# Optimization experiments

Measured on AMD Instinct MI355X. Metric: run time of the kernel, lower is better.

Reference implementation:

```python
import jax, jax.numpy as jnp
import numpy as np

EPS = 1e-12  # torch F.normalize clamps the norm at 1e-12

def _l2norm(v, axis):
    n = jnp.sqrt(jnp.sum(v * v, axis=axis, keepdims=True))
    return v / jnp.maximum(n, EPS)

def setup_inputs() -> dict:
    key = jax.random.key(0)
    k1, k2, k3, k4 = jax.random.split(key, 4)
    N, C, H, W, K = 64, 64, 64, 64, 128
    alpha = 1.0
    x = jax.random.normal(k1, (N, C, H, W), dtype=jnp.float32)
    centroids = jax.random.uniform(k2, (K, C), dtype=jnp.float32)
    # conv is initialized from centroids (2*alpha*c, -alpha*||c||) but is an
    # independent parameter after init; keep the init relationship for realism.
    conv_w = 2.0 * alpha * centroids
    conv_b = -alpha * jnp.sqrt(jnp.sum(centroids * centroids, axis=1))
    return {"x": x, "centroids": centroids, "conv_w": conv_w, "conv_b": conv_b}

def reference(x, centroids, conv_w, conv_b):
    N, C, H, W = x.shape
    K = centroids.shape[0]
    # L2-normalize descriptors along channel dim
    xn = _l2norm(x, axis=1)                                   # [N,C,H,W]
    # 1x1 conv == per-pixel linear map C->K
    logits = jnp.einsum('nchw,kc->nkhw', xn, conv_w) + conv_b[None, :, None, None]
    sa = jax.nn.softmax(logits.reshape(N, K, H * W), axis=1)  # [N,K,HW]
    xf = xn.reshape(N, C, H * W)                              # [N,C,HW]
    # vlad[n,k,c] = sum_l sa[n,k,l] * (xf[n,c,l] - centroids[k,c])
    #            = (sa @ xf^T)[n,k,c] - sum_l sa[n,k,l] * centroids[k,c]
    vlad = jnp.einsum('nkl,ncl->nkc', sa, xf) - sa.sum(axis=-1)[:, :, None] * centroids[None]
    vlad = _l2norm(vlad, axis=2)            # intra-normalization per cluster
    vlad = vlad.reshape(N, K * C)
    vlad = _l2norm(vlad, axis=1)            # global L2 normalization
    return vlad
```

## Files before the change

### kernel.cpp

```cpp
#include <hip/hip_runtime.h>
#include <math.h>

#define NIMG   64
#define CDIM   64
#define HWPX   4096
#define PARTS  8
#define KCL    128
#define PIXPART (HWPX / PARTS)
#define TL     32
#define NCHUNK (PIXPART / TL)
#define SHIFT  10.0f

#define XP_S 72
#define XC_S 40
#define PH_S 40

typedef __attribute__((ext_vector_type(8))) short short8;
typedef __attribute__((ext_vector_type(4))) float f32x4;

#define MFMA(a, b, c) __builtin_amdgcn_mfma_f32_16x16x32_bf16((a), (b), (c), 0, 0, 0)

__device__ __forceinline__ void tsplit(float f, short& hs, short& ls) {
    unsigned u = __builtin_bit_cast(unsigned, f);
    hs = (short)(u >> 16);
    float hf = __builtin_bit_cast(float, u & 0xffff0000u);
    ls = (short)(__builtin_bit_cast(unsigned, f - hf) >> 16);
}

__global__ __launch_bounds__(256, 2)
void netvlad_main(const float* __restrict__ x,
                  const float* __restrict__ conv_w,
                  const float* __restrict__ conv_b,
                  float* __restrict__ vout,
                  float* __restrict__ asout,
                  int use_atomic)
{
    __shared__ __align__(16) short xp_hi[TL * XP_S],  xp_lo[TL * XP_S];
    __shared__ __align__(16) short xc_hi[CDIM * XC_S], xc_lo[CDIM * XC_S];
    __shared__ __align__(16) short ph_hi[KCL * PH_S],  ph_lo[KCL * PH_S];
    __shared__ __align__(16) float redA[TL * 4];
    __shared__ float sumP[4 * TL];

    const int t   = threadIdx.x;
    const int w   = t >> 6;
    const int l   = t & 63;
    const int l15 = l & 15, l4 = l >> 4;
    const int n    = blockIdx.x >> 3;
    const int part = blockIdx.x & 7;
    const int p_s  = t & 31;
    const int sg   = t >> 5;

    short8 wh[2][2], wl[2][2];
    #pragma unroll
    for (int kt = 0; kt < 2; ++kt) {
        const int krow = (2 * w + kt) * 16 + l15;
        #pragma unroll
        for (int ks = 0; ks < 2; ++ks) {
            const float4* wp = (const float4*)(conv_w + krow * CDIM + ks * 32 + l4 * 8);
            float4 wa = wp[0], wb = wp[1];
            float wv[8] = {wa.x, wa.y, wa.z, wa.w, wb.x, wb.y, wb.z, wb.w};
            #pragma unroll
            for (int j = 0; j < 8; ++j) {
                short hs, ls; tsplit(wv[j], hs, ls);
                wh[kt][ks][j] = hs; wl[kt][ks][j] = ls;
            }
        }
    }
    float cbr[2][4];
    #pragma unroll
    for (int kt = 0; kt < 2; ++kt)
        #pragma unroll
        for (int i = 0; i < 4; ++i)
            cbr[kt][i] = conv_b[(2 * w + kt) * 16 + l4 * 4 + i] - SHIFT;

    f32x4 acc2[2][4];
    #pragma unroll
    for (int a = 0; a < 2; ++a)
        #pragma unroll
        for (int b = 0; b < 4; ++b) acc2[a][b] = (f32x4)0.0f;
    float asr[2][4];
    #pragma unroll
    for (int a = 0; a < 2; ++a)
        #pragma unroll
        for (int i = 0; i < 4; ++i) asr[a][i] = 0.f;

    const float* xbase = x + (size_t)n * CDIM * HWPX + part * PIXPART;

    float xv[8];
    #pragma unroll
    for (int j = 0; j < 8; ++j)
        xv[j] = xbase[(sg * 8 + j) * HWPX + p_s];

    for (int ch = 0; ch < NCHUNK; ++ch) {
        float ssq = 0.f;
        #pragma unroll
        for (int j = 0; j < 8; ++j) ssq += xv[j] * xv[j];
        ssq += __shfl_xor(ssq, 32);
        if (l < 32) redA[p_s * 4 + w] = ssq;

        short8 vh, vl;
        #pragma unroll
        for (int j = 0; j < 8; ++j) {
            short hs, ls; tsplit(xv[j], hs, ls);
            vh[j] = hs; vl[j] = ls;
            xc_hi[(sg * 8 + j) * XC_S + p_s] = hs;
            xc_lo[(sg * 8 + j) * XC_S + p_s] = ls;
        }
        *(short8*)&xp_hi[p_s * XP_S + sg * 8] = vh;
        *(short8*)&xp_lo[p_s * XP_S + sg * 8] = vl;
        __syncthreads();

        if (ch + 1 < NCHUNK) {
            #pragma unroll
            for (int j = 0; j < 8; ++j)
                xv[j] = xbase[(sg * 8 + j) * HWPX + (ch + 1) * TL + p_s];
        }

        f32x4 a1[2][2];
        #pragma unroll
        for (int a = 0; a < 2; ++a)
            #pragma unroll
            for (int b = 0; b < 2; ++b) a1[a][b] = (f32x4)0.0f;
        #pragma unroll
        for (int ks = 0; ks < 2; ++ks) {
            #pragma unroll
            for (int pt = 0; pt < 2; ++pt) {
                short8 bh = *(short8*)&xp_hi[(pt * 16 + l15) * XP_S + ks * 32 + l4 * 8];
                short8 bl = *(short8*)&xp_lo[(pt * 16 + l15) * XP_S + ks * 32 + l4 * 8];
                #pragma unroll
                for (int kt = 0; kt < 2; ++kt) {
                    a1[kt][pt] = MFMA(wh[kt][ks], bh, a1[kt][pt]);
                    a1[kt][pt] = MFMA(wh[kt][ks], bl, a1[kt][pt]);
                    a1[kt][pt] = MFMA(wl[kt][ks], bh, a1[kt][pt]);
                }
            }
        }

        float rn[2];
        #pragma unroll
        for (int pt = 0; pt < 2; ++pt) {
            float4 r4 = *(const float4*)&redA[(pt * 16 + l15) * 4];
            rn[pt] = 1.0f / fmaxf(sqrtf((r4.x + r4.y) + (r4.z + r4.w)), 1e-12f);
        }

        float e[2][2][4], sp[2] = {0.f, 0.f};
        #pragma unroll
        for (int kt = 0; kt < 2; ++kt)
            #pragma unroll
            for (int pt = 0; pt < 2; ++pt)
                #pragma unroll
                for (int i = 0; i < 4; ++i) {
                    float ev = __expf(fmaf(a1[kt][pt][i], rn[pt], cbr[kt][i]));
                    e[kt][pt][i] = ev;
                    sp[pt] += ev;
                }
        #pragma unroll
        for (int pt = 0; pt < 2; ++pt) {
            sp[pt] += __shfl_xor(sp[pt], 16);
            sp[pt] += __shfl_xor(sp[pt], 32);
        }
        if (l4 == 0) {
            sumP[w * TL + l15]      = sp[0];
            sumP[w * TL + 16 + l15] = sp[1];
        }
        __syncthreads();

        float rden[2], rdn2[2];
        #pragma unroll
        for (int pt = 0; pt < 2; ++pt) {
            const int col = pt * 16 + l15;
            float den = sumP[col] + sumP[TL + col] + sumP[2 * TL + col] + sumP[3 * TL + col];
            rden[pt] = 1.0f / den;
            rdn2[pt] = rden[pt] * rn[pt];
        }

        #pragma unroll
        for (int kt = 0; kt < 2; ++kt)
            #pragma unroll
            for (int i = 0; i < 4; ++i) {
                const int row = (2 * w + kt) * 16 + l4 * 4 + i;
                #pragma unroll
                for (int pt = 0; pt < 2; ++pt) {
                    float ev = e[kt][pt][i];
                    asr[kt][i] = fmaf(ev, rden[pt], asr[kt][i]);
                    float Pn = ev * rdn2[pt];
                    short hs, ls; tsplit(Pn, hs, ls);
                    ph_hi[row * PH_S + pt * 16 + l15] = hs;
                    ph_lo[row * PH_S + pt * 16 + l15] = ls;
                }
            }
        __syncthreads();

        {
            short8 xh2[4], xl2[4];
            #pragma unroll
            for (int ct = 0; ct < 4; ++ct) {
                xh2[ct] = *(short8*)&xc_hi[(ct * 16 + l15) * XC_S + l4 * 8];
                xl2[ct] = *(short8*)&xc_lo[(ct * 16 + l15) * XC_S + l4 * 8];
            }
            #pragma unroll
            for (int kt = 0; kt < 2; ++kt) {
                short8 ah = *(short8*)&ph_hi[((2 * w + kt) * 16 + l15) * PH_S + l4 * 8];
                short8 al = *(short8*)&ph_lo[((2 * w + kt) * 16 + l15) * PH_S + l4 * 8];
                #pragma unroll
                for (int ct = 0; ct < 4; ++ct) {
                    acc2[kt][ct] = MFMA(ah, xh2[ct], acc2[kt][ct]);
                    acc2[kt][ct] = MFMA(ah, xl2[ct], acc2[kt][ct]);
                    acc2[kt][ct] = MFMA(al, xh2[ct], acc2[kt][ct]);
                }
            }
        }
        __syncthreads();
    }

    float* vg = use_atomic ? vout + (size_t)n * KCL * CDIM
                           : vout + (size_t)(n * PARTS + part) * KCL * CDIM;
    #pragma unroll
    for (int kt = 0; kt < 2; ++kt)
        #pragma unroll
        for (int ct = 0; ct < 4; ++ct)
            #pragma unroll
            for (int i = 0; i < 4; ++i) {
                const int row = (2 * w + kt) * 16 + l4 * 4 + i;
                const int col = ct * 16 + l15;
                if (use_atomic) atomicAdd(&vg[row * CDIM + col], acc2[kt][ct][i]);
                else            vg[row * CDIM + col] = acc2[kt][ct][i];
            }

    #pragma unroll
    for (int kt = 0; kt < 2; ++kt)
        #pragma unroll
        for (int i = 0; i < 4; ++i) {
            float v = asr[kt][i];
            v += __shfl_xor(v, 1); v += __shfl_xor(v, 2);
            v += __shfl_xor(v, 4); v += __shfl_xor(v, 8);
            if (l15 == 0) {
                const int row = (2 * w + kt) * 16 + l4 * 4 + i;
                if (use_atomic) atomicAdd(&asout[n * KCL + row], v);
                else            asout[(n * PARTS + part) * KCL + row] = v;
            }
        }
}

__global__ __launch_bounds__(1024)
void netvlad_finalize(const float* __restrict__ vpart,
                      const float* __restrict__ aspart,
                      const float* __restrict__ cent,
                      float* __restrict__ out,
                      int nparts)
{
    __shared__ float wred[16];
    __shared__ float gsh;

    const int t = threadIdx.x;
    const int n = blockIdx.x;
    const int k = t >> 3, c0 = (t & 7) * 8;
    const int w2 = t >> 6;

    float vsum[8];
    #pragma unroll
    for (int j = 0; j < 8; ++j) vsum[j] = 0.f;
    float av = 0.f;
    for (int pt = 0; pt < nparts; ++pt) {
        const float* vg = vpart + (((size_t)n * nparts + pt) * KCL + k) * CDIM + c0;
        float4 a = *(const float4*)&vg[0];
        float4 b = *(const float4*)&vg[4];
        vsum[0] += a.x; vsum[1] += a.y; vsum[2] += a.z; vsum[3] += a.w;
        vsum[4] += b.x; vsum[5] += b.y; vsum[6] += b.z; vsum[7] += b.w;
        av += aspart[(n * nparts + pt) * KCL + k];
    }

    const float* cg = cent + k * CDIM + c0;
    float4 ca = *(const float4*)&cg[0];
    float4 cb4 = *(const float4*)&cg[4];
    float cc[8] = {ca.x, ca.y, ca.z, ca.w, cb4.x, cb4.y, cb4.z, cb4.w};
    float ss = 0.f;
    #pragma unroll
    for (int j = 0; j < 8; ++j) {
        vsum[j] -= av * cc[j];
        ss += vsum[j] * vsum[j];
    }
    ss += __shfl_xor(ss, 1); ss += __shfl_xor(ss, 2); ss += __shfl_xor(ss, 4);
    const float rinv = 1.0f / fmaxf(sqrtf(ss), 1e-12f);

    float contrib = ss * rinv * rinv * 0.125f;
    #pragma unroll
    for (int off = 1; off < 64; off <<= 1) contrib += __shfl_xor(contrib, off);
    if ((t & 63) == 0) wred[w2] = contrib;
    __syncthreads();
    if (t == 0) {
        float g = 0.f;
        #pragma unroll
        for (int j = 0; j < 16; ++j) g += wred[j];
        gsh = 1.0f / fmaxf(sqrtf(g), 1e-12f);
    }
    __syncthreads();

    const float s = rinv * gsh;
    float* og = out + (size_t)n * KCL * CDIM + k * CDIM + c0;
    float4 o0, o1;
    o0.x = vsum[0] * s; o0.y = vsum[1] * s; o0.z = vsum[2] * s; o0.w = vsum[3] * s;
    o1.x = vsum[4] * s; o1.y = vsum[5] * s; o1.z = vsum[6] * s; o1.w = vsum[7] * s;
    *(float4*)&og[0] = o0;
    *(float4*)&og[4] = o1;
}

extern "C" void kernel_launch(void* const* d_in, const int* in_sizes, int n_in,
                              void* d_out, int out_size, void* d_ws, size_t ws_size,
                              hipStream_t stream) {
    const float* x     = (const float*)d_in[0];
    const float* cent  = (const float*)d_in[1];
    const float* convw = (const float*)d_in[2];
    const float* convb = (const float*)d_in[3];
    float* out = (float*)d_out;

    const size_t needP = (size_t)NIMG * PARTS * (KCL * CDIM + KCL) * sizeof(float);
    int nparts, use_atomic;
    if (ws_size >= needP) { nparts = PARTS; use_atomic = 0; }
    else                  { nparts = 1;     use_atomic = 1; }

    float* vws  = (float*)d_ws;
    float* asws = vws + (size_t)NIMG * nparts * KCL * CDIM;
    if (use_atomic) {
        const size_t zb = (size_t)NIMG * (KCL * CDIM + KCL) * sizeof(float);
        hipMemsetAsync(d_ws, 0, zb, stream);
    }

    netvlad_main<<<dim3(NIMG * PARTS), dim3(256), 0, stream>>>(x, convw, convb, vws, asws, use_atomic);
    netvlad_finalize<<<dim3(NIMG), dim3(1024), 0, stream>>>(vws, asws, cent, out, nparts);
}
```

Baseline: 136.7 us.

## Split main kernel across eight waves per block and simplify finalize normalization

The main kernel now launches 512 threads per block, and each wave owns a single 16-cluster tile instead of two. Channel loads per thread are halved, and the cross-wave reductions widen to eight partial sums. This raises per-block parallelism and cuts register pressure, at the cost of doing twice as many per-chunk syncs and LDS reductions in total. The finalize kernel is split into eight blocks per image and drops the global L2 reduction. It relies on the fact that every intra-normalized cluster row has unit norm, so the global scale is the constant 1/sqrt(128). That constant is wrong only if a cluster vector is exactly zero.

```diff
diff --git a/kernel.cpp b/kernel.cpp
--- a/kernel.cpp
+++ b/kernel.cpp
@@ -10,12 +10,14 @@
 #define TL     32
 #define NCHUNK (PIXPART / TL)
 #define SHIFT  10.0f
+#define RSQRT128 0.08838834764831845f
 
 #define XP_S 72
 #define XC_S 40
 #define PH_S 40
 
 typedef __attribute__((ext_vector_type(8))) short short8;
+typedef __attribute__((ext_vector_type(4))) short short4v;
 typedef __attribute__((ext_vector_type(4))) float f32x4;
 
 #define MFMA(a, b, c) __builtin_amdgcn_mfma_f32_16x16x32_bf16((a), (b), (c), 0, 0, 0)
@@ -27,7 +29,7 @@
     ls = (short)(__builtin_bit_cast(unsigned, f - hf) >> 16);
 }
 
-__global__ __launch_bounds__(256, 2)
+__global__ __launch_bounds__(512, 4)
 void netvlad_main(const float* __restrict__ x,
                   const float* __restrict__ conv_w,
                   const float* __restrict__ conv_b,
@@ -38,8 +40,8 @@
     __shared__ __align__(16) short xp_hi[TL * XP_S],  xp_lo[TL * XP_S];
     __shared__ __align__(16) short xc_hi[CDIM * XC_S], xc_lo[CDIM * XC_S];
     __shared__ __align__(16) short ph_hi[KCL * PH_S],  ph_lo[KCL * PH_S];
-    __shared__ __align__(16) float redA[TL * 4];
-    __shared__ float sumP[4 * TL];
+    __shared__ __align__(16) float redA[TL * 8];
+    __shared__ __align__(16) float sumP[TL * 8];
 
     const int t   = threadIdx.x;
     const int w   = t >> 6;
@@ -50,10 +52,9 @@
     const int p_s  = t & 31;
     const int sg   = t >> 5;
 
-    short8 wh[2][2], wl[2][2];
-    #pragma unroll
-    for (int kt = 0; kt < 2; ++kt) {
-        const int krow = (2 * w + kt) * 16 + l15;
+    short8 wh[2], wl[2];
+    {
+        const int krow = w * 16 + l15;
         #pragma unroll
         for (int ks = 0; ks < 2; ++ks) {
             const float4* wp = (const float4*)(conv_w + krow * CDIM + ks * 32 + l4 * 8);
@@ -62,152 +63,133 @@
             #pragma unroll
             for (int j = 0; j < 8; ++j) {
                 short hs, ls; tsplit(wv[j], hs, ls);
-                wh[kt][ks][j] = hs; wl[kt][ks][j] = ls;
-            }
-        }
-    }
-    float cbr[2][4];
-    #pragma unroll
-    for (int kt = 0; kt < 2; ++kt)
-        #pragma unroll
-        for (int i = 0; i < 4; ++i)
-            cbr[kt][i] = conv_b[(2 * w + kt) * 16 + l4 * 4 + i] - SHIFT;
-
-    f32x4 acc2[2][4];
-    #pragma unroll
-    for (int a = 0; a < 2; ++a)
-        #pragma unroll
-        for (int b = 0; b < 4; ++b) acc2[a][b] = (f32x4)0.0f;
-    float asr[2][4];
-    #pragma unroll
-    for (int a = 0; a < 2; ++a)
-        #pragma unroll
-        for (int i = 0; i < 4; ++i) asr[a][i] = 0.f;
+                wh[ks][j] = hs; wl[ks][j] = ls;
+            }
+        }
+    }
+    float cbr[4];
+    #pragma unroll
+    for (int i = 0; i < 4; ++i)
+        cbr[i] = conv_b[w * 16 + l4 * 4 + i] - SHIFT;
+
+    f32x4 acc2[4];
+    #pragma unroll
+    for (int b = 0; b < 4; ++b) acc2[b] = (f32x4)0.0f;
+    float asr[4] = {0.f, 0.f, 0.f, 0.f};
 
     const float* xbase = x + (size_t)n * CDIM * HWPX + part * PIXPART;
 
-    float xv[8];
-    #pragma unroll
-    for (int j = 0; j < 8; ++j)
-        xv[j] = xbase[(sg * 8 + j) * HWPX + p_s];
+    float xv[4];
+    #pragma unroll
+    for (int j = 0; j < 4; ++j)
+        xv[j] = xbase[(sg * 4 + j) * HWPX + p_s];
 
     for (int ch = 0; ch < NCHUNK; ++ch) {
         float ssq = 0.f;
         #pragma unroll
-        for (int j = 0; j < 8; ++j) ssq += xv[j] * xv[j];
+        for (int j = 0; j < 4; ++j) ssq += xv[j] * xv[j];
         ssq += __shfl_xor(ssq, 32);
-        if (l < 32) redA[p_s * 4 + w] = ssq;
-
-        short8 vh, vl;
-        #pragma unroll
-        for (int j = 0; j < 8; ++j) {
-            short hs, ls; tsplit(xv[j], hs, ls);
-            vh[j] = hs; vl[j] = ls;
-            xc_hi[(sg * 8 + j) * XC_S + p_s] = hs;
-            xc_lo[(sg * 8 + j) * XC_S + p_s] = ls;
-        }
-        *(short8*)&xp_hi[p_s * XP_S + sg * 8] = vh;
-        *(short8*)&xp_lo[p_s * XP_S + sg * 8] = vl;
+        if (l < 32) redA[p_s * 8 + w] = ssq;
+
+        {
+            short4v vh, vl;
+            #pragma unroll
+            for (int j = 0; j < 4; ++j) {
+                short hs, ls; tsplit(xv[j], hs, ls);
+                vh[j] = hs; vl[j] = ls;
+                xc_hi[(sg * 4 + j) * XC_S + p_s] = hs;
+                xc_lo[(sg * 4 + j) * XC_S + p_s] = ls;
+            }
+            *(short4v*)&xp_hi[p_s * XP_S + sg * 4] = vh;
+            *(short4v*)&xp_lo[p_s * XP_S + sg * 4] = vl;
+        }
         __syncthreads();
 
         if (ch + 1 < NCHUNK) {
             #pragma unroll
-            for (int j = 0; j < 8; ++j)
-                xv[j] = xbase[(sg * 8 + j) * HWPX + (ch + 1) * TL + p_s];
-        }
-
-        f32x4 a1[2][2];
-        #pragma unroll
-        for (int a = 0; a < 2; ++a)
-            #pragma unroll
-            for (int b = 0; b < 2; ++b) a1[a][b] = (f32x4)0.0f;
+            for (int j = 0; j < 4; ++j)
+                xv[j] = xbase[(sg * 4 + j) * HWPX + (ch + 1) * TL + p_s];
+        }
+
+        f32x4 a1[2];
+        a1[0] = (f32x4)0.0f; a1[1] = (f32x4)0.0f;
         #pragma unroll
         for (int ks = 0; ks < 2; ++ks) {
             #pragma unroll
             for (int pt = 0; pt < 2; ++pt) {
                 short8 bh = *(short8*)&xp_hi[(pt * 16 + l15) * XP_S + ks * 32 + l4 * 8];
                 short8 bl = *(short8*)&xp_lo[(pt * 16 + l15) * XP_S + ks * 32 + l4 * 8];
-                #pragma unroll
-                for (int kt = 0; kt < 2; ++kt) {
-                    a1[kt][pt] = MFMA(wh[kt][ks], bh, a1[kt][pt]);
-                    a1[kt][pt] = MFMA(wh[kt][ks], bl, a1[kt][pt]);
-                    a1[kt][pt] = MFMA(wl[kt][ks], bh, a1[kt][pt]);
-                }
+                a1[pt] = MFMA(wh[ks], bh, a1[pt]);
+                a1[pt] = MFMA(wh[ks], bl, a1[pt]);
+                a1[pt] = MFMA(wl[ks], bh, a1[pt]);
             }
         }
 
         float rn[2];
         #pragma unroll
         for (int pt = 0; pt < 2; ++pt) {
-            float4 r4 = *(const float4*)&redA[(pt * 16 + l15) * 4];
-            rn[pt] = 1.0f / fmaxf(sqrtf((r4.x + r4.y) + (r4.z + r4.w)), 1e-12f);
-        }
-
-        float e[2][2][4], sp[2] = {0.f, 0.f};
-        #pragma unroll
-        for (int kt = 0; kt < 2; ++kt)
-            #pragma unroll
-            for (int pt = 0; pt < 2; ++pt)
-                #pragma unroll
-                for (int i = 0; i < 4; ++i) {
-                    float ev = __expf(fmaf(a1[kt][pt][i], rn[pt], cbr[kt][i]));
-                    e[kt][pt][i] = ev;
-                    sp[pt] += ev;
-                }
+            const float4* r = (const float4*)&redA[(pt * 16 + l15) * 8];
+            float4 r0 = r[0], r1 = r[1];
+            rn[pt] = 1.0f / fmaxf(sqrtf((r0.x + r0.y) + (r0.z + r0.w)
+                                      + (r1.x + r1.y) + (r1.z + r1.w)), 1e-12f);
+        }
+
+        float e[2][4], sp[2] = {0.f, 0.f};
+        #pragma unroll
+        for (int pt = 0; pt < 2; ++pt)
+            #pragma unroll
+            for (int i = 0; i < 4; ++i) {
+                float ev = __expf(fmaf(a1[pt][i], rn[pt], cbr[i]));
+                e[pt][i] = ev;
+                sp[pt] += ev;
+            }
         #pragma unroll
         for (int pt = 0; pt < 2; ++pt) {
             sp[pt] += __shfl_xor(sp[pt], 16);
             sp[pt] += __shfl_xor(sp[pt], 32);
         }
         if (l4 == 0) {
-            sumP[w * TL + l15]      = sp[0];
-            sumP[w * TL + 16 + l15] = sp[1];
+            sumP[l15 * 8 + w]        = sp[0];
+            sumP[(16 + l15) * 8 + w] = sp[1];
         }
         __syncthreads();
 
         float rden[2], rdn2[2];
         #pragma unroll
         for (int pt = 0; pt < 2; ++pt) {
-            const int col = pt * 16 + l15;
-            float den = sumP[col] + sumP[TL + col] + sumP[2 * TL + col] + sumP[3 * TL + col];
+            const float4* r = (const float4*)&sumP[(pt * 16 + l15) * 8];
+            float4 r0 = r[0], r1 = r[1];
+            float den = (r0.x + r0.y) + (r0.z + r0.w)
+                      + (r1.x + r1.y) + (r1.z + r1.w);
             rden[pt] = 1.0f / den;
             rdn2[pt] = rden[pt] * rn[pt];
         }
 
         #pragma unroll
-        for (int kt = 0; kt < 2; ++kt)
-            #pragma unroll
-            for (int i = 0; i < 4; ++i) {
-                const int row = (2 * w + kt) * 16 + l4 * 4 + i;
-                #pragma unroll
-                for (int pt = 0; pt < 2; ++pt) {
-                    float ev = e[kt][pt][i];
-                    asr[kt][i] = fmaf(ev, rden[pt], asr[kt][i]);
-                    float Pn = ev * rdn2[pt];
-                    short hs, ls; tsplit(Pn, hs, ls);
-                    ph_hi[row * PH_S + pt * 16 + l15] = hs;
-                    ph_lo[row * PH_S + pt * 16 + l15] = ls;
-                }
-            }
+        for (int i = 0; i < 4; ++i) {
+            const int row = w * 16 + l4 * 4 + i;
+            #pragma unroll
+            for (int pt = 0; pt < 2; ++pt) {
+                float ev = e[pt][i];
+                asr[i] = fmaf(ev, rden[pt], asr[i]);
+                float Pn = ev * rdn2[pt];
+                short hs, ls; tsplit(Pn, hs, ls);
+                ph_hi[row * PH_S + pt * 16 + l15] = hs;
+                ph_lo[row * PH_S + pt * 16 + l15] = ls;
+            }
+        }
         __syncthreads();
 
         {
-            short8 xh2[4], xl2[4];
+            short8 ah = *(short8*)&ph_hi[(w * 16 + l15) * PH_S + l4 * 8];
+            short8 al = *(short8*)&ph_lo[(w * 16 + l15) * PH_S + l4 * 8];
             #pragma unroll
             for (int ct = 0; ct < 4; ++ct) {
-                xh2[ct] = *(short8*)&xc_hi[(ct * 16 + l15) * XC_S + l4 * 8];
-                xl2[ct] = *(short8*)&xc_lo[(ct * 16 + l15) * XC_S + l4 * 8];
-            }
-            #pragma unroll
-            for (int kt = 0; kt < 2; ++kt) {
-                short8 ah = *(short8*)&ph_hi[((2 * w + kt) * 16 + l15) * PH_S + l4 * 8];
-                short8 al = *(short8*)&ph_lo[((2 * w + kt) * 16 + l15) * PH_S + l4 * 8];
-                #pragma unroll
-                for (int ct = 0; ct < 4; ++ct) {
-                    acc2[kt][ct] = MFMA(ah, xh2[ct], acc2[kt][ct]);
-                    acc2[kt][ct] = MFMA(ah, xl2[ct], acc2[kt][ct]);
-                    acc2[kt][ct] = MFMA(al, xh2[ct], acc2[kt][ct]);
-                }
+                short8 xh2 = *(short8*)&xc_hi[(ct * 16 + l15) * XC_S + l4 * 8];
+                short8 xl2 = *(short8*)&xc_lo[(ct * 16 + l15) * XC_S + l4 * 8];
+                acc2[ct] = MFMA(ah, xh2, acc2[ct]);
+                acc2[ct] = MFMA(ah, xl2, acc2[ct]);
+                acc2[ct] = MFMA(al, xh2, acc2[ct]);
             }
         }
         __syncthreads();
@@ -216,93 +198,65 @@
     float* vg = use_atomic ? vout + (size_t)n * KCL * CDIM
                            : vout + (size_t)(n * PARTS + part) * KCL * CDIM;
     #pragma unroll
-    for (int kt = 0; kt < 2; ++kt)
-        #pragma unroll
-        for (int ct = 0; ct < 4; ++ct)
-            #pragma unroll
-            for (int i = 0; i < 4; ++i) {
-                const int row = (2 * w + kt) * 16 + l4 * 4 + i;
-                const int col = ct * 16 + l15;
-                if (use_atomic) atomicAdd(&vg[row * CDIM + col], acc2[kt][ct][i]);
-                else            vg[row * CDIM + col] = acc2[kt][ct][i];
-            }
-
-    #pragma unroll
-    for (int kt = 0; kt < 2; ++kt)
+    for (int ct = 0; ct < 4; ++ct)
         #pragma unroll
         for (int i = 0; i < 4; ++i) {
-            float v = asr[kt][i];
-            v += __shfl_xor(v, 1); v += __shfl_xor(v, 2);
-            v += __shfl_xor(v, 4); v += __shfl_xor(v, 8);
-            if (l15 == 0) {
-                const int row = (2 * w + kt) * 16 + l4 * 4 + i;
-                if (use_atomic) atomicAdd(&asout[n * KCL + row], v);
-                else            asout[(n * PARTS + part) * KCL + row] = v;
-            }
-        }
-}
-
-__global__ __launch_bounds__(1024)
+            const int row = w * 16 + l4 * 4 + i;
+            const int col = ct * 16 + l15;
+            if (use_atomic) atomicAdd(&vg[row * CDIM + col], acc2[ct][i]);
+            else            vg[row * CDIM + col] = acc2[ct][i];
+        }
+
+    #pragma unroll
+    for (int i = 0; i < 4; ++i) {
+        float v = asr[i];
+        v += __shfl_xor(v, 1); v += __shfl_xor(v, 2);
+        v += __shfl_xor(v, 4); v += __shfl_xor(v, 8);
+        if (l15 == 0) {
+            const int row = w * 16 + l4 * 4 + i;
+            if (use_atomic) atomicAdd(&asout[n * KCL + row], v);
+            else            asout[(n * PARTS + part) * KCL + row] = v;
+        }
+    }
+}
+
+__global__ __launch_bounds__(256)
 void netvlad_finalize(const float* __restrict__ vpart,
                       const float* __restrict__ aspart,
                       const float* __restrict__ cent,
                       float* __restrict__ out,
                       int nparts)
 {
-    __shared__ float wred[16];
-    __shared__ float gsh;
-
     const int t = threadIdx.x;
-    const int n = blockIdx.x;
-    const int k = t >> 3, c0 = (t & 7) * 8;
-    const int w2 = t >> 6;
-
-    float vsum[8];
-    #pragma unroll
-    for (int j = 0; j < 8; ++j) vsum[j] = 0.f;
+    const int n  = blockIdx.x >> 3;
+    const int kg = blockIdx.x & 7;
+    const int k  = kg * 16 + (t >> 4);
+    const int c0 = (t & 15) * 4;
+
+    float vsum[4] = {0.f, 0.f, 0.f, 0.f};
     float av = 0.f;
     for (int pt = 0; pt < nparts; ++pt) {
         const float* vg = vpart + (((size_t)n * nparts + pt) * KCL + k) * CDIM + c0;
-        float4 a = *(const float4*)&vg[0];
-        float4 b = *(const float4*)&vg[4];
+        float4 a = *(const float4*)vg;
         vsum[0] += a.x; vsum[1] += a.y; vsum[2] += a.z; vsum[3] += a.w;
-        vsum[4] += b.x; vsum[5] += b.y; vsum[6] += b.z; vsum[7] += b.w;
         av += aspart[(n * nparts + pt) * KCL + k];
     }
 
-    const float* cg = cent + k * CDIM + c0;
-    float4 ca = *(const float4*)&cg[0];
-    float4 cb4 = *(const float4*)&cg[4];
-    float cc[8] = {ca.x, ca.y, ca.z, ca.w, cb4.x, cb4.y, cb4.z, cb4.w};
+    float4 cq = *(const float4*)(cent + k * CDIM + c0);
+    float cc[4] = {cq.x, cq.y, cq.z, cq.w};
     float ss = 0.f;
     #pragma unroll
-    for (int j = 0; j < 8; ++j) {
+    for (int j = 0; j < 4; ++j) {
         vsum[j] -= av * cc[j];
         ss += vsum[j] * vsum[j];
     }
-    ss += __shfl_xor(ss, 1); ss += __shfl_xor(ss, 2); ss += __shfl_xor(ss, 4);
-    const float rinv = 1.0f / fmaxf(sqrtf(ss), 1e-12f);
-
-    float contrib = ss * rinv * rinv * 0.125f;
-    #pragma unroll
-    for (int off = 1; off < 64; off <<= 1) contrib += __shfl_xor(contrib, off);
-    if ((t & 63) == 0) wred[w2] = contrib;
-    __syncthreads();
-    if (t == 0) {
-        float g = 0.f;
-        #pragma unroll
-        for (int j = 0; j < 16; ++j) g += wred[j];
-        gsh = 1.0f / fmaxf(sqrtf(g), 1e-12f);
-    }
-    __syncthreads();
-
-    const float s = rinv * gsh;
-    float* og = out + (size_t)n * KCL * CDIM + k * CDIM + c0;
-    float4 o0, o1;
-    o0.x = vsum[0] * s; o0.y = vsum[1] * s; o0.z = vsum[2] * s; o0.w = vsum[3] * s;
-    o1.x = vsum[4] * s; o1.y = vsum[5] * s; o1.z = vsum[6] * s; o1.w = vsum[7] * s;
-    *(float4*)&og[0] = o0;
-    *(float4*)&og[4] = o1;
+    ss += __shfl_xor(ss, 1); ss += __shfl_xor(ss, 2);
+    ss += __shfl_xor(ss, 4); ss += __shfl_xor(ss, 8);
+    const float s = (1.0f / fmaxf(sqrtf(ss), 1e-12f)) * RSQRT128;
+
+    float4 o;
+    o.x = vsum[0] * s; o.y = vsum[1] * s; o.z = vsum[2] * s; o.w = vsum[3] * s;
+    *(float4*)(out + (size_t)n * KCL * CDIM + k * CDIM + c0) = o;
 }
 
 extern "C" void kernel_launch(void* const* d_in, const int* in_sizes, int n_in,
@@ -326,6 +280,6 @@
         hipMemsetAsync(d_ws, 0, zb, stream);
     }
 
-    netvlad_main<<<dim3(NIMG * PARTS), dim3(256), 0, stream>>>(x, convw, convb, vws, asws, use_atomic);
-    netvlad_finalize<<<dim3(NIMG), dim3(1024), 0, stream>>>(vws, asws, cent, out, nparts);
-}
+    netvlad_main<<<dim3(NIMG * PARTS), dim3(512), 0, stream>>>(x, convw, convb, vws, asws, use_atomic);
+    netvlad_finalize<<<dim3(NIMG * 8), dim3(256), 0, stream>>>(vws, asws, cent, out, nparts);
+}
```

New measurement: 139.9 us. 2.3% more time.

## Fuse finalize into main kernel via last-block counter and constant global norm

Applied to the files above, without the earlier changes.

A per-image atomic counter lets the last of the eight partial blocks for an image sum the partial VLAD and soft-assignment results. That block then subtracts the centroid term, intra-normalizes and writes the output, so the separate finalize launch is dropped on the default workspace path. The global L2 normalization is replaced by a constant 1/sqrt(128), since every intra-normalized cluster has unit norm. In exchange, a counter memset is added each call, one block per image does the whole reduction serially, and the constant is wrong for clusters whose residual is exactly zero.

```diff
diff --git a/kernel.cpp b/kernel.cpp
--- a/kernel.cpp
+++ b/kernel.cpp
@@ -10,6 +10,7 @@
 #define TL     32
 #define NCHUNK (PIXPART / TL)
 #define SHIFT  10.0f
+#define RSQRT128 0.08838834764831845f
 
 #define XP_S 72
 #define XC_S 40
@@ -31,8 +32,11 @@
 void netvlad_main(const float* __restrict__ x,
                   const float* __restrict__ conv_w,
                   const float* __restrict__ conv_b,
+                  const float* __restrict__ cent,
                   float* __restrict__ vout,
                   float* __restrict__ asout,
+                  int* __restrict__ counters,
+                  float* __restrict__ out,
                   int use_atomic)
 {
     __shared__ __align__(16) short xp_hi[TL * XP_S],  xp_lo[TL * XP_S];
@@ -40,6 +44,7 @@
     __shared__ __align__(16) short ph_hi[KCL * PH_S],  ph_lo[KCL * PH_S];
     __shared__ __align__(16) float redA[TL * 4];
     __shared__ float sumP[4 * TL];
+    __shared__ int   is_last;
 
     const int t   = threadIdx.x;
     const int w   = t >> 6;
@@ -240,69 +245,90 @@
                 else            asout[(n * PARTS + part) * KCL + row] = v;
             }
         }
+
+    if (use_atomic) return;
+
+    __threadfence();
+    if (t == 0)
+        is_last = (atomicAdd(&counters[n], 1) == PARTS - 1);
+    __syncthreads();
+    if (!is_last) return;
+    __threadfence();
+
+    {
+        const int k = t >> 1, c0 = (t & 1) * 32;
+        float vsum[32];
+        #pragma unroll
+        for (int j = 0; j < 32; ++j) vsum[j] = 0.f;
+        float av = 0.f;
+        for (int pt = 0; pt < PARTS; ++pt) {
+            const float* vp = vout + (((size_t)n * PARTS + pt) * KCL + k) * CDIM + c0;
+            #pragma unroll
+            for (int g = 0; g < 8; ++g) {
+                float4 vq = *(const float4*)&vp[4 * g];
+                vsum[4 * g + 0] += vq.x; vsum[4 * g + 1] += vq.y;
+                vsum[4 * g + 2] += vq.z; vsum[4 * g + 3] += vq.w;
+            }
+            av += asout[(n * PARTS + pt) * KCL + k];
+        }
+        const float* cg = cent + k * CDIM + c0;
+        float ss = 0.f;
+        #pragma unroll
+        for (int g = 0; g < 8; ++g) {
+            float4 cq = *(const float4*)&cg[4 * g];
+            float r0 = vsum[4 * g + 0] - av * cq.x;
+            float r1 = vsum[4 * g + 1] - av * cq.y;
+            float r2 = vsum[4 * g + 2] - av * cq.z;
+            float r3 = vsum[4 * g + 3] - av * cq.w;
+            vsum[4 * g + 0] = r0; vsum[4 * g + 1] = r1;
+            vsum[4 * g + 2] = r2; vsum[4 * g + 3] = r3;
+            ss += r0 * r0 + r1 * r1 + r2 * r2 + r3 * r3;
+        }
+        ss += __shfl_xor(ss, 1);
+        const float s = (1.0f / fmaxf(sqrtf(ss), 1e-12f)) * RSQRT128;
+        float* og = out + (size_t)n * KCL * CDIM + k * CDIM + c0;
+        #pragma unroll
+        for (int g = 0; g < 8; ++g) {
+            float4 o;
+            o.x = vsum[4 * g + 0] * s; o.y = vsum[4 * g + 1] * s;
+            o.z = vsum[4 * g + 2] * s; o.w = vsum[4 * g + 3] * s;
+            *(float4*)&og[4 * g] = o;
+        }
+    }
 }
 
-__global__ __launch_bounds__(1024)
-void netvlad_finalize(const float* __restrict__ vpart,
-                      const float* __restrict__ aspart,
+__global__ __launch_bounds__(256)
+void netvlad_finalize(const float* __restrict__ vacc,
+                      const float* __restrict__ asum,
                       const float* __restrict__ cent,
-                      float* __restrict__ out,
-                      int nparts)
+                      float* __restrict__ out)
 {
-    __shared__ float wred[16];
-    __shared__ float gsh;
-
     const int t = threadIdx.x;
-    const int n = blockIdx.x;
-    const int k = t >> 3, c0 = (t & 7) * 8;
-    const int w2 = t >> 6;
-
-    float vsum[8];
-    #pragma unroll
-    for (int j = 0; j < 8; ++j) vsum[j] = 0.f;
-    float av = 0.f;
-    for (int pt = 0; pt < nparts; ++pt) {
-        const float* vg = vpart + (((size_t)n * nparts + pt) * KCL + k) * CDIM + c0;
-        float4 a = *(const float4*)&vg[0];
-        float4 b = *(const float4*)&vg[4];
-        vsum[0] += a.x; vsum[1] += a.y; vsum[2] += a.z; vsum[3] += a.w;
-        vsum[4] += b.x; vsum[5] += b.y; vsum[6] += b.z; vsum[7] += b.w;
-        av += aspart[(n * nparts + pt) * KCL + k];
-    }
-
-    const float* cg = cent + k * CDIM + c0;
-    float4 ca = *(const float4*)&cg[0];
-    float4 cb4 = *(const float4*)&cg[4];
-    float cc[8] = {ca.x, ca.y, ca.z, ca.w, cb4.x, cb4.y, cb4.z, cb4.w};
+    const int n  = blockIdx.x >> 3;
+    const int kg = blockIdx.x & 7;
+    const int k  = kg * 16 + (t >> 4);
+    const int c0 = (t & 15) * 4;
+
+    const float* vg = vacc + ((size_t)n * KCL + k) * CDIM + c0;
+    float4 a = *(const float4*)vg;
+    float vsum[4] = {a.x, a.y, a.z, a.w};
+    float av = asum[n * KCL + k];
+
+    float4 cq = *(const float4*)(cent + k * CDIM + c0);
+    float cc[4] = {cq.x, cq.y, cq.z, cq.w};
     float ss = 0.f;
     #pragma unroll
-    for (int j = 0; j < 8; ++j) {
+    for (int j = 0; j < 4; ++j) {
         vsum[j] -= av * cc[j];
         ss += vsum[j] * vsum[j];
     }
-    ss += __shfl_xor(ss, 1); ss += __shfl_xor(ss, 2); ss += __shfl_xor(ss, 4);
-    const float rinv = 1.0f / fmaxf(sqrtf(ss), 1e-12f);
-
-    float contrib = ss * rinv * rinv * 0.125f;
-    #pragma unroll
-    for (int off = 1; off < 64; off <<= 1) contrib += __shfl_xor(contrib, off);
-    if ((t & 63) == 0) wred[w2] = contrib;
-    __syncthreads();
-    if (t == 0) {
-        float g = 0.f;
-        #pragma unroll
-        for (int j = 0; j < 16; ++j) g += wred[j];
-        gsh = 1.0f / fmaxf(sqrtf(g), 1e-12f);
-    }
-    __syncthreads();
-
-    const float s = rinv * gsh;
-    float* og = out + (size_t)n * KCL * CDIM + k * CDIM + c0;
-    float4 o0, o1;
-    o0.x = vsum[0] * s; o0.y = vsum[1] * s; o0.z = vsum[2] * s; o0.w = vsum[3] * s;
-    o1.x = vsum[4] * s; o1.y = vsum[5] * s; o1.z = vsum[6] * s; o1.w = vsum[7] * s;
-    *(float4*)&og[0] = o0;
-    *(float4*)&og[4] = o1;
+    ss += __shfl_xor(ss, 1); ss += __shfl_xor(ss, 2);
+    ss += __shfl_xor(ss, 4); ss += __shfl_xor(ss, 8);
+    const float s = (1.0f / fmaxf(sqrtf(ss), 1e-12f)) * RSQRT128;
+
+    float4 o;
+    o.x = vsum[0] * s; o.y = vsum[1] * s; o.z = vsum[2] * s; o.w = vsum[3] * s;
+    *(float4*)(out + (size_t)n * KCL * CDIM + k * CDIM + c0) = o;
 }
 
 extern "C" void kernel_launch(void* const* d_in, const int* in_sizes, int n_in,
@@ -314,18 +340,25 @@
     const float* convb = (const float*)d_in[3];
     float* out = (float*)d_out;
 
-    const size_t needP = (size_t)NIMG * PARTS * (KCL * CDIM + KCL) * sizeof(float);
-    int nparts, use_atomic;
-    if (ws_size >= needP) { nparts = PARTS; use_atomic = 0; }
-    else                  { nparts = 1;     use_atomic = 1; }
-
-    float* vws  = (float*)d_ws;
-    float* asws = vws + (size_t)NIMG * nparts * KCL * CDIM;
-    if (use_atomic) {
+    const size_t needP = (size_t)NIMG * PARTS * (KCL * CDIM + KCL) * sizeof(float)
+                       + NIMG * sizeof(int);
+    const int use_atomic = (ws_size >= needP) ? 0 : 1;
+
+    if (!use_atomic) {
+        float* vws  = (float*)d_ws;
+        float* asws = vws + (size_t)NIMG * PARTS * KCL * CDIM;
+        int*   cnt  = (int*)(asws + (size_t)NIMG * PARTS * KCL);
+        hipMemsetAsync(cnt, 0, NIMG * sizeof(int), stream);
+        netvlad_main<<<dim3(NIMG * PARTS), dim3(256), 0, stream>>>(
+            x, convw, convb, cent, vws, asws, cnt, out, 0);
+    } else {
+        float* vws  = (float*)d_ws;
+        float* asws = vws + (size_t)NIMG * KCL * CDIM;
         const size_t zb = (size_t)NIMG * (KCL * CDIM + KCL) * sizeof(float);
         hipMemsetAsync(d_ws, 0, zb, stream);
-    }
-
-    netvlad_main<<<dim3(NIMG * PARTS), dim3(256), 0, stream>>>(x, convw, convb, vws, asws, use_atomic);
-    netvlad_finalize<<<dim3(NIMG), dim3(1024), 0, stream>>>(vws, asws, cent, out, nparts);
+        netvlad_main<<<dim3(NIMG * PARTS), dim3(256), 0, stream>>>(
+            x, convw, convb, cent, vws, asws, nullptr, out, 1);
+        netvlad_finalize<<<dim3(NIMG * 8), dim3(256), 0, stream>>>(
+            vws, asws, cent, out);
+    }
 }
```

Measured after the change: 217.7 us. 1.59x slower.
